# Kernel optimization log

Measured on AMD Instinct MI355X. Metric: run time of the kernel, lower is better.

The kernel has to match this reference:

```python
import jax, jax.numpy as jnp
import numpy as np

B, S, H, E, I, K = 1, 4096, 1024, 16, 512, 2
ISH = 1024  # shared expert intermediate = moe_intermediate_size * num_shared_experts
ROUTE_SCALE = 1.0
WSCALE = 0.02


def setup_inputs() -> dict:
    key = jax.random.key(0)
    ks = jax.random.split(key, 9)
    return {
        "hidden_states": jax.random.normal(ks[0], (B, S, H), dtype=jnp.float32),
        "router_w": jax.random.normal(ks[1], (H, E), dtype=jnp.float32) * WSCALE,
        "expert_bias": jnp.zeros((E,), dtype=jnp.float32),
        "w_gate": jax.random.normal(ks[2], (E, H, I), dtype=jnp.float32) * WSCALE,
        "w_up": jax.random.normal(ks[3], (E, H, I), dtype=jnp.float32) * WSCALE,
        "w_down": jax.random.normal(ks[4], (E, I, H), dtype=jnp.float32) * WSCALE,
        "sw_gate": jax.random.normal(ks[5], (H, ISH), dtype=jnp.float32) * WSCALE,
        "sw_up": jax.random.normal(ks[6], (H, ISH), dtype=jnp.float32) * WSCALE,
        "sw_down": jax.random.normal(ks[7], (ISH, H), dtype=jnp.float32) * WSCALE,
    }


def reference(hidden_states, router_w, expert_bias, w_gate, w_up, w_down, sw_gate, sw_up, sw_down):
    b, s, h = hidden_states.shape
    T = b * s
    xf = hidden_states.reshape(T, h)

    # --- token-choice router (sigmoid scores, top-k, normalize, scale) ---
    scores = jax.nn.sigmoid((xf @ router_w).astype(jnp.float32))          # [T, E]
    _, sel = jax.lax.top_k(scores + expert_bias[None, :], K)              # [T, K] int32
    top = jnp.take_along_axis(scores, sel, axis=1)                        # [T, K]
    top = top / (top.sum(axis=-1, keepdims=True) + 1e-20)
    top = top * ROUTE_SCALE

    # combine weights: [T, E], zero for unselected experts
    comb = jnp.zeros((T, E), jnp.float32).at[jnp.arange(T)[:, None], sel].add(top)

    # --- routed experts: SwiGLU MLP per expert (stacked weights) ---
    g = jnp.einsum('th,ehi->eti', xf, w_gate)                             # [E, T, I]
    u = jnp.einsum('th,ehi->eti', xf, w_up)                               # [E, T, I]
    a = jax.nn.silu(g) * u                                                # [E, T, I]
    eo = jnp.einsum('eti,eih->eth', a, w_down)                            # [E, T, H]
    routed = jnp.einsum('eth,te->th', eo.astype(jnp.float32), comb).astype(hidden_states.dtype)

    # --- shared experts (always active) ---
    shared = (jax.nn.silu(xf @ sw_gate) * (xf @ sw_up)) @ sw_down         # [T, H]

    return (shared + routed).reshape(b, s, h)
```

## Files before the change

### kernel.cpp

```cpp
#include <hip/hip_runtime.h>
#include <math.h>

#define T_TOK 4096
#define HDIM  1024
#define NEXP  16
#define IDIM  512
#define NSLOT 16384
#define NGRP  18
#define MAXRB 80

typedef unsigned int u32;
typedef unsigned short u16;
typedef __attribute__((ext_vector_type(8))) short bfrag;
typedef __attribute__((ext_vector_type(4))) float f32x4;

__device__ __forceinline__ u16 f2bf(float f) {
    union { float f; u32 u; } c; c.f = f;
    u32 u = c.u;
    u32 r = u + 0x7fffu + ((u >> 16) & 1u);
    return (u16)(r >> 16);
}
__device__ __forceinline__ float bf2f(u16 h) {
    union { u32 u; float f; } c; c.u = ((u32)h) << 16;
    return c.f;
}

__device__ __forceinline__ void async16(void* lds, const void* g) {
    __builtin_amdgcn_global_load_lds((__attribute__((address_space(1))) void*)(g),
                                     (__attribute__((address_space(3))) void*)(lds),
                                     16, 0, 0);
}

#define SYNCN(n) do { \
    asm volatile("s_waitcnt vmcnt(" #n ")" ::: "memory"); \
    __builtin_amdgcn_s_barrier(); \
    __builtin_amdgcn_sched_barrier(0); \
} while (0)
#define BAR2() do { \
    __builtin_amdgcn_s_barrier(); \
    __builtin_amdgcn_sched_barrier(0); \
} while (0)

__global__ __launch_bounds__(256) void cvt_f32_bf16(const float* __restrict__ src,
                                                    u16* __restrict__ dst, int n) {
    int i = (blockIdx.x * 256 + threadIdx.x) * 4;
    if (i >= n) return;
    float4 v = *(const float4*)(src + i);
    ushort4 o;
    o.x = f2bf(v.x); o.y = f2bf(v.y); o.z = f2bf(v.z); o.w = f2bf(v.w);
    *(ushort4*)(dst + i) = o;
}

__global__ __launch_bounds__(256) void transpose_k2(const float* __restrict__ src,
                                                    u16* __restrict__ dst,
                                                    int R, int C, long bstride) {
    __shared__ u16 tileT[32][132];
    long base = (long)blockIdx.z * bstride;
    int c0 = blockIdx.x * 32, r0 = blockIdx.y * 128;
    int t = threadIdx.x;
    int rr = t >> 3;
    int c4 = (t & 7) * 4;
#pragma unroll
    for (int p = 0; p < 4; ++p) {
        int r = p * 32 + rr;
        float4 v = *(const float4*)(src + base + (long)(r0 + r) * C + c0 + c4);
        tileT[c4 + 0][r] = f2bf(v.x);
        tileT[c4 + 1][r] = f2bf(v.y);
        tileT[c4 + 2][r] = f2bf(v.z);
        tileT[c4 + 3][r] = f2bf(v.w);
    }
    __syncthreads();
    int cc = t >> 5;
    int r4 = (t & 31) * 4;
#pragma unroll
    for (int q = 0; q < 4; ++q) {
        int c = q * 8 + cc;
        ushort4 o;
        o.x = tileT[c][r4]; o.y = tileT[c][r4 + 1];
        o.z = tileT[c][r4 + 2]; o.w = tileT[c][r4 + 3];
        *(ushort4*)(dst + base + (long)(c0 + c) * R + r0 + r4) = o;
    }
}

__global__ __launch_bounds__(256) void router_k(const float* __restrict__ x,
                                                const float* __restrict__ rw,
                                                const float* __restrict__ bias,
                                                int* __restrict__ sel,
                                                float* __restrict__ wts) {
    int tid = threadIdx.x;
    int wv = tid >> 6;
    int lane = tid & 63;
    int t = blockIdx.x * 4 + wv;
    int e = lane & 15, hc = lane >> 4;
    const float* xr = x + (long)t * HDIM + hc * 256;
    const float* rp = rw + (long)hc * 256 * NEXP + e;
    float acc = 0.f;
#pragma unroll 4
    for (int i = 0; i < 64; ++i) {
        float4 xv = *(const float4*)(xr + i * 4);
        acc += xv.x * rp[(i * 4 + 0) * NEXP] + xv.y * rp[(i * 4 + 1) * NEXP]
             + xv.z * rp[(i * 4 + 2) * NEXP] + xv.w * rp[(i * 4 + 3) * NEXP];
    }
    acc += __shfl_down(acc, 16);
    acc += __shfl_down(acc, 32);
    float sc = 1.f / (1.f + __expf(-acc));
    float v = sc + bias[e];
    int i0 = -1, i1 = -1;
    float v0 = -1e30f, v1 = -1e30f, s0 = 0.f, s1 = 0.f;
#pragma unroll
    for (int j = 0; j < 16; ++j) {
        float vj = __shfl(v, j);
        float scj = __shfl(sc, j);
        if (vj > v0) { v1 = v0; i1 = i0; s1 = s0; v0 = vj; i0 = j; s0 = scj; }
        else if (vj > v1) { v1 = vj; i1 = j; s1 = scj; }
    }
    if (lane == 0) {
        float nrm = s0 + s1 + 1e-20f;
        sel[t * 2] = i0; sel[t * 2 + 1] = i1;
        wts[t * 2] = s0 / nrm; wts[t * 2 + 1] = s1 / nrm;
    }
}

__global__ __launch_bounds__(1024) void route_build_k(const int* __restrict__ sel,
                                                      int* __restrict__ offs,
                                                      int* __restrict__ rowmap,
                                                      int* __restrict__ invmap,
                                                      int* __restrict__ rbGroup,
                                                      int* __restrict__ rbRow0) {
    __shared__ int hist[NEXP];
    __shared__ int cur[NEXP];
    int tid = threadIdx.x;
    if (tid < NEXP) hist[tid] = 0;
    __syncthreads();
    for (int i = tid; i < T_TOK * 2; i += 1024)
        atomicAdd(&hist[sel[i]], 1);
    __syncthreads();
    if (tid == 0) {
        int a = 0;
        for (int g = 0; g < NEXP; ++g) { cur[g] = a; offs[g] = a; a += hist[g]; }
        offs[16] = 8192;
        offs[17] = 8192 + T_TOK;
        offs[18] = 8192 + 2 * T_TOK;
        int rb = 0;
        for (int g = 0; g < NGRP; ++g)
            for (int r0 = offs[g]; r0 < offs[g + 1]; r0 += 256) {
                rbGroup[rb] = g; rbRow0[rb] = r0; ++rb;
            }
        for (; rb < MAXRB; ++rb) rbGroup[rb] = -1;
    }
    __syncthreads();
    for (int i = tid; i < T_TOK * 2; i += 1024) {
        int g = sel[i];
        int slot = atomicAdd(&cur[g], 1);
        rowmap[slot] = i >> 1;
        invmap[i] = slot;
    }
    for (int i = tid; i < T_TOK; i += 1024) {
        rowmap[8192 + i] = i;
        rowmap[8192 + T_TOK + i] = i;
    }
}

__global__ __launch_bounds__(512)
void gemm_gu(const u16* __restrict__ A,
             const u16* __restrict__ WG,
             const u16* __restrict__ WU,
             const u16* __restrict__ SWG,
             const u16* __restrict__ SWU,
             u16* __restrict__ H,
             const int* __restrict__ offs,
             const int* __restrict__ rowmap,
             const int* __restrict__ rbGroup,
             const int* __restrict__ rbRow0) {
    int rb = blockIdx.y;
    int g = rbGroup[rb];
    if (g < 0) return;
    int row0 = rbRow0[rb];
    int mend = offs[g + 1];
    int col0 = blockIdx.x * 128;
    long wb = (long)((g < 16) ? g : (g - 16)) * IDIM * HDIM;
    const u16* Bg = (g < 16) ? WG + wb : SWG + wb;
    const u16* Bu = (g < 16) ? WU + wb : SWU + wb;

    __shared__ u16 sA[2][256 * 64];
    __shared__ u16 sBg[2][128 * 64];
    __shared__ u16 sBu[2][128 * 64];

    int tid = threadIdx.x;
    int lane = tid & 63;
    int w = tid >> 6;
    int wr = (w >> 1) * 64;
    int wc = (w & 1) * 64;
    int lhi = lane >> 4, llo = lane & 15;
    int swz = llo & 7;

    const u16* pA[4]; int dA[4];
#pragma unroll
    for (int c = 0; c < 4; ++c) {
        int idx = c * 512 + tid;
        int r = idx >> 3, ch = idx & 7;
        int grow = row0 + r;
        int ar = rowmap[(grow < mend) ? grow : row0];
        pA[c] = A + (long)ar * HDIM + ((ch ^ (r & 7)) * 8);
        dA[c] = idx * 8;
    }
    const u16* pBg[2]; const u16* pBu[2]; int dB[2];
#pragma unroll
    for (int c = 0; c < 2; ++c) {
        int idx = c * 512 + tid;
        int r = idx >> 3, ch = idx & 7;
        long boff = (long)(col0 + r) * HDIM + ((ch ^ (r & 7)) * 8);
        pBg[c] = Bg + boff; pBu[c] = Bu + boff;
        dB[c] = idx * 8;
    }

    f32x4 accg[4][4], accu[4][4];
#pragma unroll
    for (int m = 0; m < 4; ++m)
#pragma unroll
        for (int n = 0; n < 4; ++n) {
            f32x4 z = {0.f, 0.f, 0.f, 0.f};
            accg[m][n] = z; accu[m][n] = z;
        }

    auto STAGE = [&](int buf) {
#pragma unroll
        for (int c = 0; c < 4; ++c) { async16(&sA[buf][dA[c]], pA[c]); pA[c] += 64; }
#pragma unroll
        for (int c = 0; c < 2; ++c) {
            async16(&sBg[buf][dB[c]], pBg[c]); pBg[c] += 64;
            async16(&sBu[buf][dB[c]], pBu[c]); pBu[c] += 64;
        }
    };
    auto COMPUTE = [&](int buf) {
#pragma unroll
        for (int kk = 0; kk < 2; ++kk) {
            int p = ((kk * 4 + lhi) ^ swz) * 8;
            bfrag a[4], bg[4], bu[4];
#pragma unroll
            for (int m = 0; m < 4; ++m)
                a[m] = *(const bfrag*)&sA[buf][(wr + m * 16 + llo) * 64 + p];
#pragma unroll
            for (int n = 0; n < 4; ++n) {
                bg[n] = *(const bfrag*)&sBg[buf][(wc + n * 16 + llo) * 64 + p];
                bu[n] = *(const bfrag*)&sBu[buf][(wc + n * 16 + llo) * 64 + p];
            }
#pragma unroll
            for (int m = 0; m < 4; ++m)
#pragma unroll
                for (int n = 0; n < 4; ++n) {
                    accg[m][n] = __builtin_amdgcn_mfma_f32_16x16x32_bf16(a[m], bg[n], accg[m][n], 0, 0, 0);
                    accu[m][n] = __builtin_amdgcn_mfma_f32_16x16x32_bf16(a[m], bu[n], accu[m][n], 0, 0, 0);
                }
        }
    };

    STAGE(0);
#pragma unroll 1
    for (int t = 0; t < 14; t += 2) {
        STAGE(1); SYNCN(8); COMPUTE(0); BAR2();
        STAGE(0); SYNCN(8); COMPUTE(1); BAR2();
    }
    STAGE(1); SYNCN(8); COMPUTE(0); BAR2();
    SYNCN(0); COMPUTE(1);

#pragma unroll
    for (int m = 0; m < 4; ++m) {
        int rbase = row0 + wr + m * 16 + lhi * 4;
#pragma unroll
        for (int n = 0; n < 4; ++n) {
            int col = col0 + wc + n * 16 + llo;
#pragma unroll
            for (int i = 0; i < 4; ++i) {
                int grow = rbase + i;
                if (grow >= mend) continue;
                float gv = accg[m][n][i], uv = accu[m][n][i];
                float hv = gv / (1.f + __expf(-gv)) * uv;
                H[(long)grow * IDIM + col] = f2bf(hv);
            }
        }
    }
}

__global__ __launch_bounds__(512)
void gemm_down(const u16* __restrict__ Hbuf,
               const u16* __restrict__ WD,
               const u16* __restrict__ SWD,
               u16* __restrict__ EO,
               const int* __restrict__ offs,
               const int* __restrict__ rbGroup,
               const int* __restrict__ rbRow0) {
    int rb = blockIdx.y;
    int g = rbGroup[rb];
    if (g < 0) return;
    int row0 = rbRow0[rb];
    int mend = offs[g + 1];
    int col0 = blockIdx.x * 256;
    long wb = (long)((g < 16) ? g : (g - 16)) * HDIM * IDIM;
    const u16* B = (g < 16) ? WD + wb : SWD + wb;

    __shared__ u16 sA[2][256 * 64];
    __shared__ u16 sB[2][256 * 64];

    int tid = threadIdx.x;
    int lane = tid & 63;
    int w = tid >> 6;
    int wr = (w >> 2) * 128;
    int wc = (w & 3) * 64;
    int lhi = lane >> 4, llo = lane & 15;
    int swz = llo & 7;

    const u16* pA[4]; const u16* pB[4]; int dd[4];
#pragma unroll
    for (int c = 0; c < 4; ++c) {
        int idx = c * 512 + tid;
        int r = idx >> 3, ch = idx & 7;
        int grow = row0 + r;
        int ar = (grow < mend) ? grow : row0;
        int chs = (ch ^ (r & 7)) * 8;
        pA[c] = Hbuf + (long)ar * IDIM + chs;
        pB[c] = B + (long)(col0 + r) * IDIM + chs;
        dd[c] = idx * 8;
    }

    f32x4 acc[8][4];
#pragma unroll
    for (int m = 0; m < 8; ++m)
#pragma unroll
        for (int n = 0; n < 4; ++n) { f32x4 z = {0.f, 0.f, 0.f, 0.f}; acc[m][n] = z; }

    auto STAGE = [&](int buf) {
#pragma unroll
        for (int c = 0; c < 4; ++c) {
            async16(&sA[buf][dd[c]], pA[c]); pA[c] += 64;
            async16(&sB[buf][dd[c]], pB[c]); pB[c] += 64;
        }
    };
    auto COMPUTE = [&](int buf) {
#pragma unroll
        for (int kk = 0; kk < 2; ++kk) {
            int p = ((kk * 4 + lhi) ^ swz) * 8;
            bfrag a[8], b[4];
#pragma unroll
            for (int m = 0; m < 8; ++m)
                a[m] = *(const bfrag*)&sA[buf][(wr + m * 16 + llo) * 64 + p];
#pragma unroll
            for (int n = 0; n < 4; ++n)
                b[n] = *(const bfrag*)&sB[buf][(wc + n * 16 + llo) * 64 + p];
#pragma unroll
            for (int m = 0; m < 8; ++m)
#pragma unroll
                for (int n = 0; n < 4; ++n)
                    acc[m][n] = __builtin_amdgcn_mfma_f32_16x16x32_bf16(a[m], b[n], acc[m][n], 0, 0, 0);
        }
    };

    STAGE(0);
#pragma unroll 1
    for (int t = 0; t < 6; t += 2) {
        STAGE(1); SYNCN(8); COMPUTE(0); BAR2();
        STAGE(0); SYNCN(8); COMPUTE(1); BAR2();
    }
    STAGE(1); SYNCN(8); COMPUTE(0); BAR2();
    SYNCN(0); COMPUTE(1);

#pragma unroll
    for (int m = 0; m < 8; ++m) {
        int rbase = row0 + wr + m * 16 + lhi * 4;
#pragma unroll
        for (int n = 0; n < 4; ++n) {
            int col = col0 + wc + n * 16 + llo;
#pragma unroll
            for (int i = 0; i < 4; ++i) {
                int grow = rbase + i;
                if (grow >= mend) continue;
                EO[(long)grow * HDIM + col] = f2bf(acc[m][n][i]);
            }
        }
    }
}

__global__ __launch_bounds__(256) void combine_k(float* __restrict__ out,
                                                 const u16* __restrict__ eo,
                                                 const int* __restrict__ invmap,
                                                 const float* __restrict__ wts) {
    int t = blockIdx.x;
    int h = threadIdx.x * 4;
    int r0 = invmap[t * 2], r1 = invmap[t * 2 + 1];
    float w0 = wts[t * 2], w1 = wts[t * 2 + 1];
    int s0 = 8192 + t, s1 = 8192 + T_TOK + t;
    ushort4 a = *(const ushort4*)(eo + (long)r0 * HDIM + h);
    ushort4 b = *(const ushort4*)(eo + (long)r1 * HDIM + h);
    ushort4 c = *(const ushort4*)(eo + (long)s0 * HDIM + h);
    ushort4 d = *(const ushort4*)(eo + (long)s1 * HDIM + h);
    float4 o;
    o.x = w0 * bf2f(a.x) + w1 * bf2f(b.x) + bf2f(c.x) + bf2f(d.x);
    o.y = w0 * bf2f(a.y) + w1 * bf2f(b.y) + bf2f(c.y) + bf2f(d.y);
    o.z = w0 * bf2f(a.z) + w1 * bf2f(b.z) + bf2f(c.z) + bf2f(d.z);
    o.w = w0 * bf2f(a.w) + w1 * bf2f(b.w) + bf2f(c.w) + bf2f(d.w);
    *(float4*)(out + (long)t * HDIM + h) = o;
}

extern "C" void kernel_launch(void* const* d_in, const int* in_sizes, int n_in,
                              void* d_out, int out_size, void* d_ws, size_t ws_size,
                              hipStream_t stream) {
    const float* x    = (const float*)d_in[0];
    const float* rw   = (const float*)d_in[1];
    const float* bias = (const float*)d_in[2];
    const float* wg   = (const float*)d_in[3];
    const float* wu   = (const float*)d_in[4];
    const float* wd   = (const float*)d_in[5];
    const float* swg  = (const float*)d_in[6];
    const float* swu  = (const float*)d_in[7];
    const float* swd  = (const float*)d_in[8];
    float* out = (float*)d_out;

    char* ws = (char*)d_ws;
    size_t o = 0;
    auto alloc = [&](size_t bytes) -> void* {
        void* p = ws + o;
        o += (bytes + 255) & ~(size_t)255;
        return p;
    };
    u16* x_bf = (u16*)alloc((size_t)T_TOK * HDIM * 2);
    u16* WtG  = (u16*)alloc((size_t)NEXP * IDIM * HDIM * 2);
    u16* WtU  = (u16*)alloc((size_t)NEXP * IDIM * HDIM * 2);
    u16* WtD  = (u16*)alloc((size_t)NEXP * HDIM * IDIM * 2);
    u16* SWtG = (u16*)alloc((size_t)2 * IDIM * HDIM * 2);
    u16* SWtU = (u16*)alloc((size_t)2 * IDIM * HDIM * 2);
    u16* SWtD = (u16*)alloc((size_t)2 * HDIM * IDIM * 2);
    u16* Hbuf = (u16*)alloc((size_t)NSLOT * IDIM * 2);
    int*   sel     = (int*)alloc((size_t)T_TOK * 2 * 4);
    float* wts     = (float*)alloc((size_t)T_TOK * 2 * 4);
    int*   invmap  = (int*)alloc((size_t)T_TOK * 2 * 4);
    int*   rowmap  = (int*)alloc((size_t)NSLOT * 4);
    int*   offs    = (int*)alloc((NGRP + 1) * 4);
    int*   rbGroup = (int*)alloc(MAXRB * 4);
    int*   rbRow0  = (int*)alloc(MAXRB * 4);
    u16* EO = WtG;

    cvt_f32_bf16<<<dim3((T_TOK * HDIM) / (4 * 256)), 256, 0, stream>>>(x, x_bf, T_TOK * HDIM);

    transpose_k2<<<dim3(IDIM / 32, HDIM / 128, NEXP), 256, 0, stream>>>(wg, WtG, HDIM, IDIM, (long)HDIM * IDIM);
    transpose_k2<<<dim3(IDIM / 32, HDIM / 128, NEXP), 256, 0, stream>>>(wu, WtU, HDIM, IDIM, (long)HDIM * IDIM);
    transpose_k2<<<dim3(HDIM / 32, IDIM / 128, NEXP), 256, 0, stream>>>(wd, WtD, IDIM, HDIM, (long)IDIM * HDIM);
    transpose_k2<<<dim3((2 * IDIM) / 32, HDIM / 128, 1), 256, 0, stream>>>(swg, SWtG, HDIM, 2 * IDIM, 0);
    transpose_k2<<<dim3((2 * IDIM) / 32, HDIM / 128, 1), 256, 0, stream>>>(swu, SWtU, HDIM, 2 * IDIM, 0);
    transpose_k2<<<dim3(HDIM / 32, IDIM / 128, 2), 256, 0, stream>>>(swd, SWtD, IDIM, HDIM, (long)IDIM * HDIM);

    router_k<<<dim3(T_TOK / 4), 256, 0, stream>>>(x, rw, bias, sel, wts);
    route_build_k<<<dim3(1), 1024, 0, stream>>>(sel, offs, rowmap, invmap, rbGroup, rbRow0);

    gemm_gu<<<dim3(IDIM / 128, MAXRB), 512, 0, stream>>>(
        x_bf, WtG, WtU, SWtG, SWtU, Hbuf, offs, rowmap, rbGroup, rbRow0);

    gemm_down<<<dim3(HDIM / 256, MAXRB), 512, 0, stream>>>(
        Hbuf, WtD, SWtD, EO, offs, rbGroup, rbRow0);

    combine_k<<<dim3(T_TOK), 256, 0, stream>>>(out, EO, invmap, wts);
}
```

Measured before the change: 182.6 us.

## Interleave LDS reads with MFMA and split staging in grouped GEMMs

Both grouped GEMM kernels now use a finer-grained software pipeline. Each k-tile is split into four phases, each with a barrier, a fragment read and an MFMA batch, and the global-to-LDS copies of the A and B tiles are issued at separate points so they overlap more compute. MFMA sections run at raised wave priority via s_setprio. The grid is flattened to 1D with a remap that spreads consecutive workgroups across XCD-like groups of 8, aiming for better cache locality. The cost is more barriers per tile and some reliance on vmcnt counts being correct for the split staging.

```diff
diff --git a/kernel.cpp b/kernel.cpp
--- a/kernel.cpp
+++ b/kernel.cpp
@@ -31,15 +31,9 @@
                                      16, 0, 0);
 }
 
-#define SYNCN(n) do { \
-    asm volatile("s_waitcnt vmcnt(" #n ")" ::: "memory"); \
-    __builtin_amdgcn_s_barrier(); \
-    __builtin_amdgcn_sched_barrier(0); \
-} while (0)
-#define BAR2() do { \
-    __builtin_amdgcn_s_barrier(); \
-    __builtin_amdgcn_sched_barrier(0); \
-} while (0)
+#define VMW(n) asm volatile("s_waitcnt vmcnt(" #n ")" ::: "memory")
+#define BARSB() do { __builtin_amdgcn_s_barrier(); __builtin_amdgcn_sched_barrier(0); } while (0)
+#define SB0()   __builtin_amdgcn_sched_barrier(0)
 
 __global__ __launch_bounds__(256) void cvt_f32_bf16(const float* __restrict__ src,
                                                     u16* __restrict__ dst, int n) {
@@ -172,12 +166,16 @@
              const int* __restrict__ rowmap,
              const int* __restrict__ rbGroup,
              const int* __restrict__ rbRow0) {
-    int rb = blockIdx.y;
+    const int NWG = 4 * MAXRB;
+    int f = blockIdx.x;
+    int L = (f & 7) * (NWG / 8) + (f >> 3);
+    int cb = L & 3;
+    int rb = L >> 2;
     int g = rbGroup[rb];
     if (g < 0) return;
     int row0 = rbRow0[rb];
     int mend = offs[g + 1];
-    int col0 = blockIdx.x * 128;
+    int col0 = cb * 128;
     long wb = (long)((g < 16) ? g : (g - 16)) * IDIM * HDIM;
     const u16* Bg = (g < 16) ? WG + wb : SWG + wb;
     const u16* Bu = (g < 16) ? WU + wb : SWU + wb;
@@ -223,46 +221,72 @@
             accg[m][n] = z; accu[m][n] = z;
         }
 
-    auto STAGE = [&](int buf) {
+    auto STAGE_A = [&](int buf) {
 #pragma unroll
         for (int c = 0; c < 4; ++c) { async16(&sA[buf][dA[c]], pA[c]); pA[c] += 64; }
+    };
+    auto STAGE_GU = [&](int buf) {
 #pragma unroll
         for (int c = 0; c < 2; ++c) {
             async16(&sBg[buf][dB[c]], pBg[c]); pBg[c] += 64;
             async16(&sBu[buf][dB[c]], pBu[c]); pBu[c] += 64;
         }
     };
-    auto COMPUTE = [&](int buf) {
-#pragma unroll
-        for (int kk = 0; kk < 2; ++kk) {
-            int p = ((kk * 4 + lhi) ^ swz) * 8;
-            bfrag a[4], bg[4], bu[4];
-#pragma unroll
-            for (int m = 0; m < 4; ++m)
-                a[m] = *(const bfrag*)&sA[buf][(wr + m * 16 + llo) * 64 + p];
-#pragma unroll
-            for (int n = 0; n < 4; ++n) {
-                bg[n] = *(const bfrag*)&sBg[buf][(wc + n * 16 + llo) * 64 + p];
-                bu[n] = *(const bfrag*)&sBu[buf][(wc + n * 16 + llo) * 64 + p];
-            }
-#pragma unroll
-            for (int m = 0; m < 4; ++m)
-#pragma unroll
-                for (int n = 0; n < 4; ++n) {
-                    accg[m][n] = __builtin_amdgcn_mfma_f32_16x16x32_bf16(a[m], bg[n], accg[m][n], 0, 0, 0);
-                    accu[m][n] = __builtin_amdgcn_mfma_f32_16x16x32_bf16(a[m], bu[n], accu[m][n], 0, 0, 0);
-                }
-        }
-    };
-
-    STAGE(0);
+
+    bfrag av[4], bv[4];
+    auto RD_A = [&](int buf, int kk) {
+        int p = ((kk * 4 + lhi) ^ swz) * 8;
+#pragma unroll
+        for (int m = 0; m < 4; ++m)
+            av[m] = *(const bfrag*)&sA[buf][(wr + m * 16 + llo) * 64 + p];
+    };
+    auto RD_BG = [&](int buf, int kk) {
+        int p = ((kk * 4 + lhi) ^ swz) * 8;
+#pragma unroll
+        for (int n = 0; n < 4; ++n)
+            bv[n] = *(const bfrag*)&sBg[buf][(wc + n * 16 + llo) * 64 + p];
+    };
+    auto RD_BU = [&](int buf, int kk) {
+        int p = ((kk * 4 + lhi) ^ swz) * 8;
+#pragma unroll
+        for (int n = 0; n < 4; ++n)
+            bv[n] = *(const bfrag*)&sBu[buf][(wc + n * 16 + llo) * 64 + p];
+    };
+    auto MM = [&](f32x4 (&ac)[4][4]) {
+        __builtin_amdgcn_s_setprio(1);
+#pragma unroll
+        for (int m = 0; m < 4; ++m)
+#pragma unroll
+            for (int n = 0; n < 4; ++n)
+                ac[m][n] = __builtin_amdgcn_mfma_f32_16x16x32_bf16(av[m], bv[n], ac[m][n], 0, 0, 0);
+        __builtin_amdgcn_s_setprio(0);
+        __builtin_amdgcn_sched_barrier(0);
+    };
+
+    const int NT = HDIM / 64;
+    STAGE_A(0); STAGE_GU(0);
 #pragma unroll 1
-    for (int t = 0; t < 14; t += 2) {
-        STAGE(1); SYNCN(8); COMPUTE(0); BAR2();
-        STAGE(0); SYNCN(8); COMPUTE(1); BAR2();
-    }
-    STAGE(1); SYNCN(8); COMPUTE(0); BAR2();
-    SYNCN(0); COMPUTE(1);
+    for (int t = 0; t < NT - 1; ++t) {
+        int cur = t & 1, nxt = cur ^ 1;
+        STAGE_A(nxt);
+        VMW(4); BARSB();
+        RD_A(cur, 0); RD_BG(cur, 0); MM(accg);
+        STAGE_GU(nxt);
+        BARSB();
+        RD_BU(cur, 0); MM(accu);
+        BARSB();
+        RD_A(cur, 1); RD_BG(cur, 1); MM(accg);
+        BARSB();
+        RD_BU(cur, 1); MM(accu);
+    }
+    {
+        int cur = (NT - 1) & 1;
+        VMW(0); BARSB();
+        RD_A(cur, 0); RD_BG(cur, 0); MM(accg);
+        RD_BU(cur, 0); MM(accu);
+        RD_A(cur, 1); RD_BG(cur, 1); MM(accg);
+        RD_BU(cur, 1); MM(accu);
+    }
 
 #pragma unroll
     for (int m = 0; m < 4; ++m) {
@@ -290,12 +314,16 @@
                const int* __restrict__ offs,
                const int* __restrict__ rbGroup,
                const int* __restrict__ rbRow0) {
-    int rb = blockIdx.y;
+    const int NWG = 4 * MAXRB;
+    int f = blockIdx.x;
+    int L = (f & 7) * (NWG / 8) + (f >> 3);
+    int cb = L & 3;
+    int rb = L >> 2;
     int g = rbGroup[rb];
     if (g < 0) return;
     int row0 = rbRow0[rb];
     int mend = offs[g + 1];
-    int col0 = blockIdx.x * 256;
+    int col0 = cb * 256;
     long wb = (long)((g < 16) ? g : (g - 16)) * HDIM * IDIM;
     const u16* B = (g < 16) ? WD + wb : SWD + wb;
 
@@ -329,40 +357,63 @@
 #pragma unroll
         for (int n = 0; n < 4; ++n) { f32x4 z = {0.f, 0.f, 0.f, 0.f}; acc[m][n] = z; }
 
-    auto STAGE = [&](int buf) {
-#pragma unroll
-        for (int c = 0; c < 4; ++c) {
-            async16(&sA[buf][dd[c]], pA[c]); pA[c] += 64;
-            async16(&sB[buf][dd[c]], pB[c]); pB[c] += 64;
-        }
-    };
-    auto COMPUTE = [&](int buf) {
-#pragma unroll
-        for (int kk = 0; kk < 2; ++kk) {
-            int p = ((kk * 4 + lhi) ^ swz) * 8;
-            bfrag a[8], b[4];
-#pragma unroll
-            for (int m = 0; m < 8; ++m)
-                a[m] = *(const bfrag*)&sA[buf][(wr + m * 16 + llo) * 64 + p];
+    auto STAGE_A = [&](int buf) {
+#pragma unroll
+        for (int c = 0; c < 4; ++c) { async16(&sA[buf][dd[c]], pA[c]); pA[c] += 64; }
+    };
+    auto STAGE_B = [&](int buf) {
+#pragma unroll
+        for (int c = 0; c < 4; ++c) { async16(&sB[buf][dd[c]], pB[c]); pB[c] += 64; }
+    };
+
+    bfrag av[4], bb[4];
+    auto RD_A = [&](int buf, int kk, int ro) {
+        int p = ((kk * 4 + lhi) ^ swz) * 8;
+#pragma unroll
+        for (int m = 0; m < 4; ++m)
+            av[m] = *(const bfrag*)&sA[buf][(wr + ro + m * 16 + llo) * 64 + p];
+    };
+    auto RD_B = [&](int buf, int kk) {
+        int p = ((kk * 4 + lhi) ^ swz) * 8;
+#pragma unroll
+        for (int n = 0; n < 4; ++n)
+            bb[n] = *(const bfrag*)&sB[buf][(wc + n * 16 + llo) * 64 + p];
+    };
+    auto MMD = [&](int mo) {
+        __builtin_amdgcn_s_setprio(1);
+#pragma unroll
+        for (int m = 0; m < 4; ++m)
 #pragma unroll
             for (int n = 0; n < 4; ++n)
-                b[n] = *(const bfrag*)&sB[buf][(wc + n * 16 + llo) * 64 + p];
-#pragma unroll
-            for (int m = 0; m < 8; ++m)
-#pragma unroll
-                for (int n = 0; n < 4; ++n)
-                    acc[m][n] = __builtin_amdgcn_mfma_f32_16x16x32_bf16(a[m], b[n], acc[m][n], 0, 0, 0);
-        }
-    };
-
-    STAGE(0);
+                acc[mo + m][n] = __builtin_amdgcn_mfma_f32_16x16x32_bf16(av[m], bb[n], acc[mo + m][n], 0, 0, 0);
+        __builtin_amdgcn_s_setprio(0);
+        __builtin_amdgcn_sched_barrier(0);
+    };
+
+    const int NT = IDIM / 64;
+    STAGE_B(0); STAGE_A(0);
 #pragma unroll 1
-    for (int t = 0; t < 6; t += 2) {
-        STAGE(1); SYNCN(8); COMPUTE(0); BAR2();
-        STAGE(0); SYNCN(8); COMPUTE(1); BAR2();
-    }
-    STAGE(1); SYNCN(8); COMPUTE(0); BAR2();
-    SYNCN(0); COMPUTE(1);
+    for (int t = 0; t < NT - 1; ++t) {
+        int cur = t & 1, nxt = cur ^ 1;
+        STAGE_B(nxt);
+        VMW(4); BARSB();
+        RD_A(cur, 0, 0); RD_B(cur, 0); MMD(0);
+        STAGE_A(nxt);
+        BARSB();
+        RD_A(cur, 0, 64); MMD(4);
+        BARSB();
+        RD_A(cur, 1, 0); RD_B(cur, 1); MMD(0);
+        BARSB();
+        RD_A(cur, 1, 64); MMD(4);
+    }
+    {
+        int cur = (NT - 1) & 1;
+        VMW(0); BARSB();
+        RD_A(cur, 0, 0); RD_B(cur, 0); MMD(0);
+        RD_A(cur, 0, 64); MMD(4);
+        RD_A(cur, 1, 0); RD_B(cur, 1); MMD(0);
+        RD_A(cur, 1, 64); MMD(4);
+    }
 
 #pragma unroll
     for (int m = 0; m < 8; ++m) {
@@ -451,10 +502,10 @@
     router_k<<<dim3(T_TOK / 4), 256, 0, stream>>>(x, rw, bias, sel, wts);
     route_build_k<<<dim3(1), 1024, 0, stream>>>(sel, offs, rowmap, invmap, rbGroup, rbRow0);
 
-    gemm_gu<<<dim3(IDIM / 128, MAXRB), 512, 0, stream>>>(
+    gemm_gu<<<dim3(4 * MAXRB), 512, 0, stream>>>(
         x_bf, WtG, WtU, SWtG, SWtU, Hbuf, offs, rowmap, rbGroup, rbRow0);
 
-    gemm_down<<<dim3(HDIM / 256, MAXRB), 512, 0, stream>>>(
+    gemm_down<<<dim3(4 * MAXRB), 512, 0, stream>>>(
         Hbuf, WtD, SWtD, EO, offs, rbGroup, rbRow0);
 
     combine_k<<<dim3(T_TOK), 256, 0, stream>>>(out, EO, invmap, wts);
```

Measured after the change: 192.2 us. +5.3%, slower.
